# Optimization experiments

Hardware: AMD Instinct MI355X
Metric: run time of the kernel (lower is better)

Reference implementation:

```python
import jax, jax.numpy as jnp
import numpy as np

N, E, D, H = 16000, 256000, 128, 4
ALPHA = 0.2  # LeakyReLU negative slope


def setup_inputs() -> dict:
    key = jax.random.key(0)
    ks = jax.random.split(key, 9)
    s = 0.1
    return {
        "h": jax.random.normal(ks[0], (N, D), jnp.float32),
        "W": jax.random.normal(ks[1], (H, D, D), jnp.float32) * s,
        "a": jax.random.normal(ks[2], (H, 2 * D), jnp.float32) * s,
        "W_ih": jax.random.normal(ks[3], (3 * D, H * D), jnp.float32) * s,
        "W_hh": jax.random.normal(ks[4], (3 * D, D), jnp.float32) * s,
        "b_ih": jnp.zeros((3 * D,), jnp.float32),
        "b_hh": jnp.zeros((3 * D,), jnp.float32),
        "src": jax.random.randint(ks[5], (E,), 0, N, jnp.int32),
        "dst": jax.random.randint(ks[6], (E,), 0, N, jnp.int32),
    }


def reference(h, W, a, W_ih, W_hh, b_ih, b_hh, src, dst):
    n = h.shape[0]
    # Per-head linear transform: Wh[n,h,d]
    Wh = jnp.einsum("nd,hde->nhe", h, W)
    a1, a2 = a[:, :D], a[:, D:]
    s_src = jnp.einsum("nhd,hd->nh", Wh, a1)  # src attention logits
    s_dst = jnp.einsum("nhd,hd->nh", Wh, a2)  # dst attention logits
    e = jax.nn.leaky_relu(s_src[src] + s_dst[dst], ALPHA)  # [E,H]
    # Segment softmax over incoming edges of each dst node
    m = jax.ops.segment_max(e, dst, num_segments=n)          # [N,H]
    ex = jnp.exp(e - m[dst])
    denom = jax.ops.segment_sum(ex, dst, num_segments=n)     # [N,H]
    att = ex / denom[dst]                                    # [E,H]
    # Weighted message aggregation: h_prime[n,h,d]
    h_prime = jax.ops.segment_sum(att[:, :, None] * Wh[src], dst, num_segments=n)
    x = h_prime.reshape(n, H * D)  # concat heads
    # PyTorch GRUCell(input=H*D, hidden=D)
    gi = x @ W_ih.T + b_ih
    gh = h @ W_hh.T + b_hh
    i_r, i_z, i_n = jnp.split(gi, 3, axis=1)
    h_r, h_z, h_n = jnp.split(gh, 3, axis=1)
    r = jax.nn.sigmoid(i_r + h_r)
    z = jax.nn.sigmoid(i_z + h_z)
    nvec = jnp.tanh(i_n + r * h_n)
    return (1.0 - z) * nvec + z * h
```

## Files before the change

kernel.cpp:

```cpp
#include <hip/hip_runtime.h>
#include <math.h>

#define N_NODES 16000
#define E_EDGES 256000
#define DIM 128
#define HEADS 4
#define LRELU_ALPHA 0.2f

typedef unsigned short u16;
typedef unsigned int u32;
typedef short bf16x8 __attribute__((ext_vector_type(8)));
typedef float floatx4 __attribute__((ext_vector_type(4)));

#define AS1 __attribute__((address_space(1)))
#define AS3 __attribute__((address_space(3)))

__device__ __forceinline__ u16 f2bf(float f) {
    u32 u = __float_as_uint(f);
    u32 r = (u + 0x7fffu + ((u >> 16) & 1u)) >> 16;
    return (u16)r;
}
__device__ __forceinline__ float bflo(u32 v) { return __uint_as_float(v << 16); }
__device__ __forceinline__ float bfhi(u32 v) { return __uint_as_float(v & 0xffff0000u); }
__device__ __forceinline__ u32 pack2(float lo, float hi) {
    return (u32)f2bf(lo) | ((u32)f2bf(hi) << 16);
}

__global__ __launch_bounds__(256) void init_kernel(
    const float* __restrict__ W, const float* __restrict__ a,
    float* __restrict__ wa1, float* __restrict__ wa2, int* __restrict__ deg)
{
    int t = blockIdx.x * blockDim.x + threadIdx.x;
    if (t <= N_NODES) deg[t] = 0;
    if (t < HEADS * DIM) {
        int h = t >> 7;
        const float* wrow = W + (long)t * DIM;
        const float* a1 = a + h * 2 * DIM;
        const float* a2 = a1 + DIM;
        float s1 = 0.f, s2 = 0.f;
        for (int e = 0; e < DIM; ++e) {
            float w = wrow[e];
            s1 = fmaf(w, a1[e], s1);
            s2 = fmaf(w, a2[e], s2);
        }
        wa1[t] = s1;
        wa2[t] = s2;
    }
}

__global__ __launch_bounds__(256) void prep_kernel(
    const float* __restrict__ hin, const float* __restrict__ wa1, const float* __restrict__ wa2,
    const float* __restrict__ W_ih, const float* __restrict__ W, const float* __restrict__ W_hh,
    const int* __restrict__ dst,
    float* __restrict__ s_src, float* __restrict__ s_dst,
    u16* __restrict__ xcat, u16* __restrict__ Wihb, u16* __restrict__ Wb,
    u16* __restrict__ Wcat, int* __restrict__ deg)
{
    const int b = blockIdx.x;
    const int tid = threadIdx.x;
    if (b < N_NODES) {
        const int n = b;
        const int hh = tid >> 6;
        const int lane = tid & 63;
        float h0 = hin[(long)n * DIM + lane];
        float h1 = hin[(long)n * DIM + 64 + lane];
        if (hh == 0) {
            xcat[(size_t)n * 640 + 512 + lane] = f2bf(h0);
            xcat[(size_t)n * 640 + 576 + lane] = f2bf(h1);
        }
        const float* w1 = wa1 + hh * DIM;
        const float* w2 = wa2 + hh * DIM;
        float p = h0 * w1[lane] + h1 * w1[64 + lane];
        float q = h0 * w2[lane] + h1 * w2[64 + lane];
        #pragma unroll
        for (int off = 32; off > 0; off >>= 1) {
            p += __shfl_down(p, off, 64);
            q += __shfl_down(q, off, 64);
        }
        if (lane == 0) { s_src[n * HEADS + hh] = p; s_dst[n * HEADS + hh] = q; }
    } else if (b < N_NODES + 1000) {
        int e = (b - N_NODES) * 256 + tid;
        atomicAdd(&deg[dst[e]], 1);
    } else if (b < N_NODES + 1768) {
        int i = (b - N_NODES - 1000) * 256 + tid;
        Wihb[i] = f2bf(W_ih[i]);
        if (i < HEADS * DIM * DIM) Wb[i] = f2bf(W[i]);
    } else {
        int t = (b - N_NODES - 1768) * 256 + tid;
        if (t < 65536) {
            int j = t >> 7, e = t & 127;
            u16 val;
            if (j < 256)      val = f2bf(W_hh[j * 128 + e]);
            else if (j < 384) val = 0;
            else              val = f2bf(W_hh[(j - 128) * 128 + e]);
            Wcat[(size_t)j * 640 + 512 + e] = val;
        } else {
            int t2 = t - 65536;
            int j = 384 + (t2 >> 9), c = t2 & 511;
            Wcat[(size_t)j * 640 + c] = 0;
        }
    }
}

__global__ __launch_bounds__(1024) void scan_kernel(const int* __restrict__ deg,
    int* __restrict__ offsets, int* __restrict__ cursor)
{
    __shared__ int wsum[16];
    const int tid = threadIdx.x;
    const int lane = tid & 63;
    const int w = tid >> 6;
    const int4* d4 = (const int4*)deg;
    int v[16];
    int tot = 0;
    #pragma unroll
    for (int i = 0; i < 4; ++i) {
        int i4 = tid * 4 + i;
        int4 vv = (i4 < N_NODES / 4) ? d4[i4] : int4{0, 0, 0, 0};
        v[i * 4 + 0] = vv.x; v[i * 4 + 1] = vv.y; v[i * 4 + 2] = vv.z; v[i * 4 + 3] = vv.w;
        tot += vv.x + vv.y + vv.z + vv.w;
    }
    int x = tot;
    #pragma unroll
    for (int off = 1; off < 64; off <<= 1) {
        int t = __shfl_up(x, off, 64);
        if (lane >= off) x += t;
    }
    if (lane == 63) wsum[w] = x;
    __syncthreads();
    if (w == 0) {
        int s = (lane < 16) ? wsum[lane] : 0;
        #pragma unroll
        for (int off = 1; off < 16; off <<= 1) {
            int t = __shfl_up(s, off, 64);
            if (lane >= off) s += t;
        }
        if (lane < 16) wsum[lane] = s;
    }
    __syncthreads();
    int excl = x - tot + ((w == 0) ? 0 : wsum[w - 1]);
    #pragma unroll
    for (int i = 0; i < 4; ++i) {
        int i4 = tid * 4 + i;
        if (i4 < N_NODES / 4) {
            int4 o;
            o.x = excl;
            o.y = excl + v[i * 4];
            o.z = o.y + v[i * 4 + 1];
            o.w = o.z + v[i * 4 + 2];
            ((int4*)offsets)[i4] = o;
            ((int4*)cursor)[i4] = o;
            excl = o.w + v[i * 4 + 3];
        }
    }
    if (tid == 1023) offsets[N_NODES] = excl;
}

__device__ __forceinline__ void gemm_tile(const u16* A, const u16* Bt, u16* C,
    int K, int lda, int ldb, int ldc, int row0, int col0, char* SMp, int tid)
{
    u16 (*Alds)[32] = (u16(*)[32])SMp;
    u16 (*Blds)[32] = (u16(*)[32])(SMp + 8192);
    const int wave = tid >> 6;
    const int lane = tid & 63;
    const int quad = lane >> 4;
    const int l15  = lane & 15;
    const int wm = (wave >> 1) * 64;
    const int wn = (wave & 1) * 64;
    const int ch0 = wave * 2;
    const int srow = lane >> 2;
    const int scol = (lane & 3) * 8;

    floatx4 acc[4][4] = {};

    for (int k0 = 0; k0 < K; k0 += 32) {
        #pragma unroll
        for (int c = 0; c < 2; ++c) {
            int ch = ch0 + c;
            const u16* ga = A + (size_t)(row0 + ch * 16 + srow) * lda + k0 + scol;
            __builtin_amdgcn_global_load_lds((AS1 void*)ga, (AS3 void*)&Alds[ch * 16][0], 16, 0, 0);
            const u16* gb = Bt + (size_t)(col0 + ch * 16 + srow) * ldb + k0 + scol;
            __builtin_amdgcn_global_load_lds((AS1 void*)gb, (AS3 void*)&Blds[ch * 16][0], 16, 0, 0);
        }
        __syncthreads();
        bf16x8 af[4], bfr[4];
        #pragma unroll
        for (int i = 0; i < 4; ++i) af[i] = *(const bf16x8*)&Alds[wm + i * 16 + l15][quad * 8];
        #pragma unroll
        for (int j = 0; j < 4; ++j) bfr[j] = *(const bf16x8*)&Blds[wn + j * 16 + l15][quad * 8];
        #pragma unroll
        for (int i = 0; i < 4; ++i)
            #pragma unroll
            for (int j = 0; j < 4; ++j)
                acc[i][j] = __builtin_amdgcn_mfma_f32_16x16x32_bf16(af[i], bfr[j], acc[i][j], 0, 0, 0);
        __syncthreads();
    }
    #pragma unroll
    for (int i = 0; i < 4; ++i) {
        #pragma unroll
        for (int r = 0; r < 4; ++r) {
            int row = row0 + wm + i * 16 + quad * 4 + r;
            size_t base = (size_t)row * ldc + col0 + wn + l15;
            #pragma unroll
            for (int j = 0; j < 4; ++j) C[base + j * 16] = f2bf(acc[i][j][r]);
        }
    }
}

__global__ __launch_bounds__(256) void scatter_mt_kernel(
    const int* __restrict__ src, const int* __restrict__ dst,
    int* __restrict__ cursor, int* __restrict__ ssorted,
    const u16* __restrict__ Wihb, const u16* __restrict__ Wb, u16* __restrict__ Wcat)
{
    __shared__ __align__(16) char SM[16384];
    const int b = blockIdx.x;
    const int tid = threadIdx.x;
    if (b < 12) {
        int y = b % 3, z = b / 3;
        gemm_tile(Wihb + z * 128, Wb + (size_t)z * 16384, Wcat + z * 128,
                  128, 512, 128, 640, y * 128, 0, SM, tid);
    } else {
        int e = (b - 12) * 256 + tid;
        int pos = atomicAdd(&cursor[dst[e]], 1);
        ssorted[pos] = src[e];
    }
}

__global__ __launch_bounds__(256) void aggregate_kernel(
    const float* __restrict__ s_src, const float* __restrict__ s_dst,
    const int* __restrict__ offs, const int* __restrict__ srcs,
    u16* __restrict__ xcat)
{
    const int tid = threadIdx.x;
    const int lane = tid & 63;
    const int n = blockIdx.x * 4 + (tid >> 6);
    const int start = offs[n];
    const int deg = offs[n + 1] - start;
    u32* xrow = (u32*)(xcat + (size_t)n * 640);
    if (deg == 0) {
        #pragma unroll
        for (int h = 0; h < 4; ++h) xrow[h * 64 + lane] = 0u;
        return;
    }
    const u32* hb = (const u32*)xcat;
    const float sd = s_dst[n * HEADS + (lane & 3)];
    const int j16 = lane >> 2;
    const int hh  = lane & 3;

    float2 acc[4] = {{0.f,0.f},{0.f,0.f},{0.f,0.f},{0.f,0.f}};
    float dsum[4] = {0.f, 0.f, 0.f, 0.f};

    for (int cb = 0; cb < deg; cb += 16) {
        const int clen = min(16, deg - cb);
        int sv = 0;
        if (lane < clen) sv = srcs[start + cb + lane];
        float wv = 0.f;
        if (j16 < clen) {
            int s = __shfl(sv, j16, 64);
            float e = s_src[s * HEADS + hh] + sd;
            e = e > 0.f ? e : LRELU_ALPHA * e;
            wv = __expf(e);
        }
        int e = 0;
        for (; e + 4 <= clen; e += 4) {
            u32 vs[4];
            #pragma unroll
            for (int k = 0; k < 4; ++k) {
                int s = __shfl(sv, e + k, 64);
                vs[k] = hb[s * 320 + 256 + lane];
            }
            #pragma unroll
            for (int k = 0; k < 4; ++k) {
                float lo = bflo(vs[k]), hi = bfhi(vs[k]);
                #pragma unroll
                for (int h = 0; h < 4; ++h) {
                    float w = __shfl(wv, (e + k) * 4 + h, 64);
                    acc[h].x = fmaf(w, lo, acc[h].x);
                    acc[h].y = fmaf(w, hi, acc[h].y);
                    dsum[h] += w;
                }
            }
        }
        for (; e < clen; ++e) {
            int s = __shfl(sv, e, 64);
            u32 v = hb[s * 320 + 256 + lane];
            float lo = bflo(v), hi = bfhi(v);
            #pragma unroll
            for (int h = 0; h < 4; ++h) {
                float w = __shfl(wv, e * 4 + h, 64);
                acc[h].x = fmaf(w, lo, acc[h].x);
                acc[h].y = fmaf(w, hi, acc[h].y);
                dsum[h] += w;
            }
        }
    }
    #pragma unroll
    for (int h = 0; h < 4; ++h) {
        float invd = 1.f / dsum[h];
        xrow[h * 64 + lane] = pack2(acc[h].x * invd, acc[h].y * invd);
    }
}

__global__ __launch_bounds__(256) void gemm_main_kernel(
    const u16* __restrict__ xcat, const u16* __restrict__ Wcat, u16* __restrict__ g)
{
    __shared__ __align__(16) char SM[16384];
    gemm_tile(xcat, Wcat, g, 640, 640, 640, 512,
              blockIdx.y * 128, blockIdx.x * 128, SM, threadIdx.x);
}

__global__ __launch_bounds__(256) void gru_kernel(const u32* __restrict__ g32,
    const float* __restrict__ b_ih, const float* __restrict__ b_hh,
    const float* __restrict__ hin, float* __restrict__ out)
{
    int p = blockIdx.x * blockDim.x + threadIdx.x;
    if (p >= N_NODES * 64) return;
    int n = p >> 6, d2 = p & 63;
    const u32* gr = g32 + (size_t)n * 256;
    u32 vr = gr[d2], vz = gr[64 + d2], vi = gr[128 + d2], vh = gr[192 + d2];
    const float2* bi2 = (const float2*)b_ih;
    const float2* bh2 = (const float2*)b_hh;
    float2 bir = bi2[d2],      bhr = bh2[d2];
    float2 biz = bi2[64 + d2], bhz = bh2[64 + d2];
    float2 bin = bi2[128 + d2], bhn = bh2[128 + d2];
    float2 hv = ((const float2*)hin)[p];
    float2 o;
    {
        float A = bflo(vr) + bir.x + bhr.x;
        float B = bflo(vz) + biz.x + bhz.x;
        float Cn = bflo(vi) + bin.x;
        float Dn = bflo(vh) + bhn.x;
        float r = 1.f / (1.f + __expf(-A));
        float z = 1.f / (1.f + __expf(-B));
        float e2 = __expf(2.f * (Cn + r * Dn));
        float nv = (e2 - 1.f) / (e2 + 1.f);
        o.x = (1.f - z) * nv + z * hv.x;
    }
    {
        float A = bfhi(vr) + bir.y + bhr.y;
        float B = bfhi(vz) + biz.y + bhz.y;
        float Cn = bfhi(vi) + bin.y;
        float Dn = bfhi(vh) + bhn.y;
        float r = 1.f / (1.f + __expf(-A));
        float z = 1.f / (1.f + __expf(-B));
        float e2 = __expf(2.f * (Cn + r * Dn));
        float nv = (e2 - 1.f) / (e2 + 1.f);
        o.y = (1.f - z) * nv + z * hv.y;
    }
    ((float2*)out)[p] = o;
}

extern "C" void kernel_launch(void* const* d_in, const int* in_sizes, int n_in,
                              void* d_out, int out_size, void* d_ws, size_t ws_size,
                              hipStream_t stream)
{
    const float* h    = (const float*)d_in[0];
    const float* W    = (const float*)d_in[1];
    const float* a    = (const float*)d_in[2];
    const float* W_ih = (const float*)d_in[3];
    const float* W_hh = (const float*)d_in[4];
    const float* b_ih = (const float*)d_in[5];
    const float* b_hh = (const float*)d_in[6];
    const int*   src  = (const int*)d_in[7];
    const int*   dst  = (const int*)d_in[8];
    float* out = (float*)d_out;

    char* ws = (char*)d_ws;
    size_t off = 0;
    auto alloc = [&](size_t bytes) { void* p = ws + off; off += (bytes + 255) & ~(size_t)255; return p; };

    u16*   xcat = (u16*)alloc((size_t)N_NODES * 640 * 2);
    u16*   g    = (u16*)alloc((size_t)N_NODES * 512 * 2);
    u16*   Wihb = (u16*)alloc(384 * 512 * 2);
    u16*   Wb   = (u16*)alloc(HEADS * 128 * 128 * 2);
    u16*   Wcat = (u16*)alloc(512 * 640 * 2);
    float* wa1  = (float*)alloc(512 * 4);
    float* wa2  = (float*)alloc(512 * 4);
    float* s_src = (float*)alloc((size_t)N_NODES * HEADS * 4);
    float* s_dst = (float*)alloc((size_t)N_NODES * HEADS * 4);
    int*   deg  = (int*)alloc((N_NODES + 1) * 4);
    int*   offs = (int*)alloc((N_NODES + 1) * 4);
    int*   cur  = (int*)alloc(N_NODES * 4);
    int*   ssort = (int*)alloc((size_t)E_EDGES * 4);

    init_kernel<<<64, 256, 0, stream>>>(W, a, wa1, wa2, deg);

    prep_kernel<<<N_NODES + 1768 + 512, 256, 0, stream>>>(
        h, wa1, wa2, W_ih, W, W_hh, dst, s_src, s_dst, xcat, Wihb, Wb, Wcat, deg);

    scan_kernel<<<1, 1024, 0, stream>>>(deg, offs, cur);

    scatter_mt_kernel<<<1012, 256, 0, stream>>>(src, dst, cur, ssort, Wihb, Wb, Wcat);

    aggregate_kernel<<<N_NODES / 4, 256, 0, stream>>>(s_src, s_dst, offs, ssort, xcat);

    gemm_main_kernel<<<dim3(4, 125), 256, 0, stream>>>(xcat, Wcat, g);

    gru_kernel<<<(N_NODES * 64 + 255) / 256, 256, 0, stream>>>(
        (const u32*)g, b_ih, b_hh, h, out);
}
```

Measured before the change: 166.3 us.

## Fuse preprocessing, histogram, scan, scatter, aggregation into one cooperative persistent kernel

```diff
diff --git a/kernel.cpp b/kernel.cpp
--- a/kernel.cpp
+++ b/kernel.cpp
@@ -1,11 +1,15 @@
 #include <hip/hip_runtime.h>
+#include <hip/hip_cooperative_groups.h>
 #include <math.h>
+
+namespace cg = cooperative_groups;
 
 #define N_NODES 16000
 #define E_EDGES 256000
 #define DIM 128
 #define HEADS 4
 #define LRELU_ALPHA 0.2f
+#define NB1 960
 
 typedef unsigned short u16;
 typedef unsigned int u32;
@@ -26,15 +30,18 @@
     return (u32)f2bf(lo) | ((u32)f2bf(hi) << 16);
 }
 
-__global__ __launch_bounds__(256) void init_kernel(
-    const float* __restrict__ W, const float* __restrict__ a,
-    float* __restrict__ wa1, float* __restrict__ wa2, int* __restrict__ deg)
-{
-    int t = blockIdx.x * blockDim.x + threadIdx.x;
-    if (t <= N_NODES) deg[t] = 0;
-    if (t < HEADS * DIM) {
-        int h = t >> 7;
-        const float* wrow = W + (long)t * DIM;
+
+__device__ __forceinline__ void pz_work(int gt, int GT,
+    const float* __restrict__ hin, const float* __restrict__ W, const float* __restrict__ a,
+    const float* __restrict__ W_ih, const float* __restrict__ W_hh,
+    u16* __restrict__ xcat, u16* __restrict__ Wihb, u16* __restrict__ Wb,
+    u16* __restrict__ Wcat, float* __restrict__ wa1, float* __restrict__ wa2,
+    int* __restrict__ deg)
+{
+    for (int i = gt; i < N_NODES + 1; i += GT) deg[i] = 0;
+    if (gt < 512) {
+        int h = gt >> 7;
+        const float* wrow = W + (long)gt * DIM;
         const float* a1 = a + h * 2 * DIM;
         const float* a2 = a1 + DIM;
         float s1 = 0.f, s2 = 0.f;
@@ -43,82 +50,72 @@
             s1 = fmaf(w, a1[e], s1);
             s2 = fmaf(w, a2[e], s2);
         }
-        wa1[t] = s1;
-        wa2[t] = s2;
-    }
-}
-
-__global__ __launch_bounds__(256) void prep_kernel(
-    const float* __restrict__ hin, const float* __restrict__ wa1, const float* __restrict__ wa2,
-    const float* __restrict__ W_ih, const float* __restrict__ W, const float* __restrict__ W_hh,
-    const int* __restrict__ dst,
-    float* __restrict__ s_src, float* __restrict__ s_dst,
-    u16* __restrict__ xcat, u16* __restrict__ Wihb, u16* __restrict__ Wb,
-    u16* __restrict__ Wcat, int* __restrict__ deg)
-{
-    const int b = blockIdx.x;
-    const int tid = threadIdx.x;
-    if (b < N_NODES) {
-        const int n = b;
-        const int hh = tid >> 6;
-        const int lane = tid & 63;
-        float h0 = hin[(long)n * DIM + lane];
-        float h1 = hin[(long)n * DIM + 64 + lane];
-        if (hh == 0) {
-            xcat[(size_t)n * 640 + 512 + lane] = f2bf(h0);
-            xcat[(size_t)n * 640 + 576 + lane] = f2bf(h1);
-        }
-        const float* w1 = wa1 + hh * DIM;
-        const float* w2 = wa2 + hh * DIM;
-        float p = h0 * w1[lane] + h1 * w1[64 + lane];
-        float q = h0 * w2[lane] + h1 * w2[64 + lane];
+        wa1[gt] = s1;
+        wa2[gt] = s2;
+    }
+    for (int i = gt; i < 384 * 512; i += GT) Wihb[i] = f2bf(W_ih[i]);
+    for (int i = gt; i < HEADS * DIM * DIM; i += GT) Wb[i] = f2bf(W[i]);
+    for (int i = gt; i < 512 * 128; i += GT) {
+        int j = i >> 7, e = i & 127;
+        u16 val;
+        if (j < 256)      val = f2bf(W_hh[j * 128 + e]);
+        else if (j < 384) val = 0;
+        else              val = f2bf(W_hh[(j - 128) * 128 + e]);
+        Wcat[(size_t)j * 640 + 512 + e] = val;
+    }
+    for (int i = gt; i < 128 * 512; i += GT) {
+        int j = 384 + (i >> 9), c = i & 511;
+        Wcat[(size_t)j * 640 + c] = 0;
+    }
+    const float2* h2 = (const float2*)hin;
+    u32* xc32 = (u32*)xcat;
+    for (int p = gt; p < N_NODES * 64; p += GT) {
+        int n = p >> 6, d = p & 63;
+        float2 hv = h2[p];
+        xc32[n * 320 + 256 + d] = pack2(hv.x, hv.y);
+    }
+}
+
+__device__ __forceinline__ void score_wave(int n, const float* __restrict__ hin,
+    const float* __restrict__ wa1, const float* __restrict__ wa2,
+    float* __restrict__ s_src, float* __restrict__ s_dst, int lane)
+{
+    float2 hv = ((const float2*)hin)[n * 64 + lane];
+    float ps[4], qs[4];
+    #pragma unroll
+    for (int h = 0; h < 4; ++h) {
+        float2 w1 = ((const float2*)(wa1 + h * 128))[lane];
+        float2 w2 = ((const float2*)(wa2 + h * 128))[lane];
+        float p = hv.x * w1.x + hv.y * w1.y;
+        float q = hv.x * w2.x + hv.y * w2.y;
         #pragma unroll
         for (int off = 32; off > 0; off >>= 1) {
-            p += __shfl_down(p, off, 64);
-            q += __shfl_down(q, off, 64);
-        }
-        if (lane == 0) { s_src[n * HEADS + hh] = p; s_dst[n * HEADS + hh] = q; }
-    } else if (b < N_NODES + 1000) {
-        int e = (b - N_NODES) * 256 + tid;
-        atomicAdd(&deg[dst[e]], 1);
-    } else if (b < N_NODES + 1768) {
-        int i = (b - N_NODES - 1000) * 256 + tid;
-        Wihb[i] = f2bf(W_ih[i]);
-        if (i < HEADS * DIM * DIM) Wb[i] = f2bf(W[i]);
-    } else {
-        int t = (b - N_NODES - 1768) * 256 + tid;
-        if (t < 65536) {
-            int j = t >> 7, e = t & 127;
-            u16 val;
-            if (j < 256)      val = f2bf(W_hh[j * 128 + e]);
-            else if (j < 384) val = 0;
-            else              val = f2bf(W_hh[(j - 128) * 128 + e]);
-            Wcat[(size_t)j * 640 + 512 + e] = val;
-        } else {
-            int t2 = t - 65536;
-            int j = 384 + (t2 >> 9), c = t2 & 511;
-            Wcat[(size_t)j * 640 + c] = 0;
-        }
-    }
-}
-
-__global__ __launch_bounds__(1024) void scan_kernel(const int* __restrict__ deg,
-    int* __restrict__ offsets, int* __restrict__ cursor)
-{
-    __shared__ int wsum[16];
-    const int tid = threadIdx.x;
-    const int lane = tid & 63;
-    const int w = tid >> 6;
+            p += __shfl_xor(p, off, 64);
+            q += __shfl_xor(q, off, 64);
+        }
+        ps[h] = p; qs[h] = q;
+    }
+    if (lane == 0) {
+        #pragma unroll
+        for (int h = 0; h < 4; ++h) {
+            s_src[n * HEADS + h] = ps[h];
+            s_dst[n * HEADS + h] = qs[h];
+        }
+    }
+}
+
+__device__ __forceinline__ void scan_block(const int* __restrict__ deg,
+    int* __restrict__ offs, int* __restrict__ cur, int tid, int* wsum)
+{
     const int4* d4 = (const int4*)deg;
-    int v[16];
     int tot = 0;
-    #pragma unroll
-    for (int i = 0; i < 4; ++i) {
-        int i4 = tid * 4 + i;
-        int4 vv = (i4 < N_NODES / 4) ? d4[i4] : int4{0, 0, 0, 0};
-        v[i * 4 + 0] = vv.x; v[i * 4 + 1] = vv.y; v[i * 4 + 2] = vv.z; v[i * 4 + 3] = vv.w;
-        tot += vv.x + vv.y + vv.z + vv.w;
-    }
+    if (tid < 250) {
+        for (int i = 0; i < 16; ++i) {
+            int4 v = d4[tid * 16 + i];
+            tot += v.x + v.y + v.z + v.w;
+        }
+    }
+    const int lane = tid & 63, w = tid >> 6;
     int x = tot;
     #pragma unroll
     for (int off = 1; off < 64; off <<= 1) {
@@ -127,32 +124,23 @@
     }
     if (lane == 63) wsum[w] = x;
     __syncthreads();
-    if (w == 0) {
-        int s = (lane < 16) ? wsum[lane] : 0;
-        #pragma unroll
-        for (int off = 1; off < 16; off <<= 1) {
-            int t = __shfl_up(s, off, 64);
-            if (lane >= off) s += t;
-        }
-        if (lane < 16) wsum[lane] = s;
-    }
-    __syncthreads();
-    int excl = x - tot + ((w == 0) ? 0 : wsum[w - 1]);
-    #pragma unroll
-    for (int i = 0; i < 4; ++i) {
-        int i4 = tid * 4 + i;
-        if (i4 < N_NODES / 4) {
+    int pre = 0;
+    for (int k = 0; k < w; ++k) pre += wsum[k];
+    int run = pre + x - tot;
+    if (tid < 250) {
+        for (int i = 0; i < 16; ++i) {
+            int4 v = d4[tid * 16 + i];
             int4 o;
-            o.x = excl;
-            o.y = excl + v[i * 4];
-            o.z = o.y + v[i * 4 + 1];
-            o.w = o.z + v[i * 4 + 2];
-            ((int4*)offsets)[i4] = o;
-            ((int4*)cursor)[i4] = o;
-            excl = o.w + v[i * 4 + 3];
-        }
-    }
-    if (tid == 1023) offsets[N_NODES] = excl;
+            o.x = run;
+            o.y = run + v.x;
+            o.z = o.y + v.y;
+            o.w = o.z + v.z;
+            ((int4*)offs)[tid * 16 + i] = o;
+            ((int4*)cur)[tid * 16 + i] = o;
+            run = o.w + v.w;
+        }
+        if (tid == 249) offs[N_NODES] = run;
+    }
 }
 
 __device__ __forceinline__ void gemm_tile(const u16* A, const u16* Bt, u16* C,
@@ -206,33 +194,11 @@
     }
 }
 
-__global__ __launch_bounds__(256) void scatter_mt_kernel(
-    const int* __restrict__ src, const int* __restrict__ dst,
-    int* __restrict__ cursor, int* __restrict__ ssorted,
-    const u16* __restrict__ Wihb, const u16* __restrict__ Wb, u16* __restrict__ Wcat)
-{
-    __shared__ __align__(16) char SM[16384];
-    const int b = blockIdx.x;
-    const int tid = threadIdx.x;
-    if (b < 12) {
-        int y = b % 3, z = b / 3;
-        gemm_tile(Wihb + z * 128, Wb + (size_t)z * 16384, Wcat + z * 128,
-                  128, 512, 128, 640, y * 128, 0, SM, tid);
-    } else {
-        int e = (b - 12) * 256 + tid;
-        int pos = atomicAdd(&cursor[dst[e]], 1);
-        ssorted[pos] = src[e];
-    }
-}
-
-__global__ __launch_bounds__(256) void aggregate_kernel(
+__device__ __forceinline__ void agg_wave(int n,
     const float* __restrict__ s_src, const float* __restrict__ s_dst,
     const int* __restrict__ offs, const int* __restrict__ srcs,
-    u16* __restrict__ xcat)
-{
-    const int tid = threadIdx.x;
-    const int lane = tid & 63;
-    const int n = blockIdx.x * 4 + (tid >> 6);
+    u16* __restrict__ xcat, int lane)
+{
     const int start = offs[n];
     const int deg = offs[n + 1] - start;
     u32* xrow = (u32*)(xcat + (size_t)n * 640);
@@ -300,6 +266,114 @@
     }
 }
 
+__global__ __launch_bounds__(256, 4) void mega_light(
+    const float* __restrict__ hin, const float* __restrict__ W, const float* __restrict__ a,
+    const float* __restrict__ W_ih, const float* __restrict__ W_hh,
+    const int* __restrict__ src, const int* __restrict__ dst,
+    u16* __restrict__ xcat, u16* __restrict__ Wihb, u16* __restrict__ Wb,
+    u16* __restrict__ Wcat,
+    float* __restrict__ wa1, float* __restrict__ wa2,
+    float* __restrict__ s_src, float* __restrict__ s_dst,
+    int* __restrict__ deg, int* __restrict__ offs, int* __restrict__ cur,
+    int* __restrict__ ssort)
+{
+    __shared__ __align__(16) char SM[16384];
+    cg::grid_group grid = cg::this_grid();
+    const int tid = threadIdx.x;
+    const int b = blockIdx.x;
+    const int NB = gridDim.x;
+    const int GT = NB * 256;
+    const int gt = b * 256 + tid;
+    const int lane = tid & 63;
+    const int wv = tid >> 6;
+
+    pz_work(gt, GT, hin, W, a, W_ih, W_hh, xcat, Wihb, Wb, Wcat, wa1, wa2, deg);
+    grid.sync();
+
+    for (int e = gt; e < E_EDGES; e += GT) atomicAdd(&deg[dst[e]], 1);
+    grid.sync();
+
+    if (b == 0) {
+        scan_block(deg, offs, cur, tid, (int*)SM);
+    } else if (b <= 12) {
+        int t = b - 1, y = t % 3, z = t / 3;
+        gemm_tile(Wihb + z * 128, Wb + (size_t)z * 16384, Wcat + z * 128,
+                  128, 512, 128, 640, y * 128, 0, SM, tid);
+    } else {
+        for (int n = (b - 13) * 4 + wv; n < N_NODES; n += (NB - 13) * 4)
+            score_wave(n, hin, wa1, wa2, s_src, s_dst, lane);
+    }
+    grid.sync();
+
+    for (int e = gt; e < E_EDGES; e += GT) {
+        int pos = atomicAdd(&cur[dst[e]], 1);
+        ssort[pos] = src[e];
+    }
+    grid.sync();
+
+    for (int n = b * 4 + wv; n < N_NODES; n += NB * 4)
+        agg_wave(n, s_src, s_dst, offs, ssort, xcat, lane);
+}
+
+__global__ __launch_bounds__(256) void k_pz(
+    const float* __restrict__ hin, const float* __restrict__ W, const float* __restrict__ a,
+    const float* __restrict__ W_ih, const float* __restrict__ W_hh,
+    u16* __restrict__ xcat, u16* __restrict__ Wihb, u16* __restrict__ Wb,
+    u16* __restrict__ Wcat, float* __restrict__ wa1, float* __restrict__ wa2,
+    int* __restrict__ deg)
+{
+    pz_work(blockIdx.x * 256 + threadIdx.x, gridDim.x * 256,
+            hin, W, a, W_ih, W_hh, xcat, Wihb, Wb, Wcat, wa1, wa2, deg);
+}
+
+__global__ __launch_bounds__(256) void k_hist(const int* __restrict__ dst, int* __restrict__ deg)
+{
+    int e = blockIdx.x * 256 + threadIdx.x;
+    if (e < E_EDGES) atomicAdd(&deg[dst[e]], 1);
+}
+
+__global__ __launch_bounds__(256) void k_scan_mt_scores(
+    const int* __restrict__ deg, int* __restrict__ offs, int* __restrict__ cur,
+    const u16* __restrict__ Wihb, const u16* __restrict__ Wb, u16* __restrict__ Wcat,
+    const float* __restrict__ hin, const float* __restrict__ wa1, const float* __restrict__ wa2,
+    float* __restrict__ s_src, float* __restrict__ s_dst)
+{
+    __shared__ __align__(16) char SM[16384];
+    const int tid = threadIdx.x;
+    const int b = blockIdx.x;
+    const int NB = gridDim.x;
+    if (b == 0) {
+        scan_block(deg, offs, cur, tid, (int*)SM);
+    } else if (b <= 12) {
+        int t = b - 1, y = t % 3, z = t / 3;
+        gemm_tile(Wihb + z * 128, Wb + (size_t)z * 16384, Wcat + z * 128,
+                  128, 512, 128, 640, y * 128, 0, SM, tid);
+    } else {
+        for (int n = (b - 13) * 4 + (tid >> 6); n < N_NODES; n += (NB - 13) * 4)
+            score_wave(n, hin, wa1, wa2, s_src, s_dst, tid & 63);
+    }
+}
+
+__global__ __launch_bounds__(256) void k_scatter(
+    const int* __restrict__ src, const int* __restrict__ dst,
+    int* __restrict__ cur, int* __restrict__ ssort)
+{
+    int e = blockIdx.x * 256 + threadIdx.x;
+    if (e < E_EDGES) {
+        int pos = atomicAdd(&cur[dst[e]], 1);
+        ssort[pos] = src[e];
+    }
+}
+
+__global__ __launch_bounds__(256) void k_agg(
+    const float* __restrict__ s_src, const float* __restrict__ s_dst,
+    const int* __restrict__ offs, const int* __restrict__ srcs,
+    u16* __restrict__ xcat)
+{
+    agg_wave(blockIdx.x * 4 + (threadIdx.x >> 6), s_src, s_dst, offs, srcs, xcat,
+             threadIdx.x & 63);
+}
+
 __global__ __launch_bounds__(256) void gemm_main_kernel(
     const u16* __restrict__ xcat, const u16* __restrict__ Wcat, u16* __restrict__ g)
 {
@@ -312,15 +386,15 @@
     const float* __restrict__ b_ih, const float* __restrict__ b_hh,
     const float* __restrict__ hin, float* __restrict__ out)
 {
-    int p = blockIdx.x * blockDim.x + threadIdx.x;
+    int p = blockIdx.x * 256 + threadIdx.x;
     if (p >= N_NODES * 64) return;
     int n = p >> 6, d2 = p & 63;
     const u32* gr = g32 + (size_t)n * 256;
     u32 vr = gr[d2], vz = gr[64 + d2], vi = gr[128 + d2], vh = gr[192 + d2];
     const float2* bi2 = (const float2*)b_ih;
     const float2* bh2 = (const float2*)b_hh;
-    float2 bir = bi2[d2],      bhr = bh2[d2];
-    float2 biz = bi2[64 + d2], bhz = bh2[64 + d2];
+    float2 bir = bi2[d2],       bhr = bh2[d2];
+    float2 biz = bi2[64 + d2],  bhz = bh2[64 + d2];
     float2 bin = bi2[128 + d2], bhn = bh2[128 + d2];
     float2 hv = ((const float2*)hin)[p];
     float2 o;
@@ -371,7 +445,7 @@
     u16*   xcat = (u16*)alloc((size_t)N_NODES * 640 * 2);
     u16*   g    = (u16*)alloc((size_t)N_NODES * 512 * 2);
     u16*   Wihb = (u16*)alloc(384 * 512 * 2);
-    u16*   Wb   = (u16*)alloc(HEADS * 128 * 128 * 2);
+    u16*   Wb   = (u16*)alloc(HEADS * DIM * DIM * 2);
     u16*   Wcat = (u16*)alloc(512 * 640 * 2);
     float* wa1  = (float*)alloc(512 * 4);
     float* wa2  = (float*)alloc(512 * 4);
@@ -382,19 +456,26 @@
     int*   cur  = (int*)alloc(N_NODES * 4);
     int*   ssort = (int*)alloc((size_t)E_EDGES * 4);
 
-    init_kernel<<<64, 256, 0, stream>>>(W, a, wa1, wa2, deg);
-
-    prep_kernel<<<N_NODES + 1768 + 512, 256, 0, stream>>>(
-        h, wa1, wa2, W_ih, W, W_hh, dst, s_src, s_dst, xcat, Wihb, Wb, Wcat, deg);
-
-    scan_kernel<<<1, 1024, 0, stream>>>(deg, offs, cur);
-
-    scatter_mt_kernel<<<1012, 256, 0, stream>>>(src, dst, cur, ssort, Wihb, Wb, Wcat);
-
-    aggregate_kernel<<<N_NODES / 4, 256, 0, stream>>>(s_src, s_dst, offs, ssort, xcat);
+    void* args1[] = {
+        (void*)&h, (void*)&W, (void*)&a, (void*)&W_ih, (void*)&W_hh,
+        (void*)&src, (void*)&dst,
+        (void*)&xcat, (void*)&Wihb, (void*)&Wb, (void*)&Wcat,
+        (void*)&wa1, (void*)&wa2, (void*)&s_src, (void*)&s_dst,
+        (void*)&deg, (void*)&offs, (void*)&cur, (void*)&ssort
+    };
+    hipError_t err = hipLaunchCooperativeKernel((const void*)mega_light,
+                                                dim3(NB1), dim3(256), args1, 0, stream);
+    if (err != hipSuccess) {
+        (void)hipGetLastError();
+        k_pz<<<960, 256, 0, stream>>>(h, W, a, W_ih, W_hh, xcat, Wihb, Wb, Wcat, wa1, wa2, deg);
+        k_hist<<<1000, 256, 0, stream>>>(dst, deg);
+        k_scan_mt_scores<<<960, 256, 0, stream>>>(deg, offs, cur, Wihb, Wb, Wcat,
+                                                  h, wa1, wa2, s_src, s_dst);
+        k_scatter<<<1000, 256, 0, stream>>>(src, dst, cur, ssort);
+        k_agg<<<N_NODES / 4, 256, 0, stream>>>(s_src, s_dst, offs, ssort, xcat);
+    }
 
     gemm_main_kernel<<<dim3(4, 125), 256, 0, stream>>>(xcat, Wcat, g);
-
     gru_kernel<<<(N_NODES * 64 + 255) / 256, 256, 0, stream>>>(
         (const u32*)g, b_ih, b_hh, h, out);
 }
```

New measurement: 625.3 us. +276.1%, slower.
